# Optimization experiments

Measured on AMD Instinct MI355X. Metric: run time of the kernel, lower is better.

## Reference

```python
import jax, jax.numpy as jnp
import numpy as np

A = 180      # number of projection angles (theta = arange(180))
STEPS = 4    # partial-sum bands -> output has 1+STEPS channels


def _radon(x):
    # x: [N, 1, W, W]
    N, C, H, W = x.shape
    img = x[:, 0]  # [N, W, W]

    # --- affine grids for all angles (torch affine_grid, align_corners=False) ---
    thetas = jnp.arange(A, dtype=jnp.float32) * (jnp.pi / 180.0)
    c = jnp.cos(thetas)[:, None, None]   # [A,1,1]
    s = jnp.sin(thetas)[:, None, None]
    # align_corners=False base coords: centers of pixels in [-1, 1]
    base = ((jnp.arange(W, dtype=jnp.float32) + 0.5) * (2.0 / W)) - 1.0
    bx = base[None, None, :]             # [1,1,W] (x varies along last dim)
    by = base[None, :, None]             # [1,W,1] (y varies along rows)
    # R = [[cos, sin, 0], [-sin, cos, 0]]
    gx = c * bx + s * by                 # [A,W,W] normalized sample x
    gy = -s * bx + c * by                # [A,W,W] normalized sample y

    # --- bilinear grid_sample, padding_mode='zeros', align_corners=False ---
    ix = ((gx + 1.0) * W - 1.0) * 0.5
    iy = ((gy + 1.0) * W - 1.0) * 0.5
    x0 = jnp.floor(ix).astype(jnp.int32); x1 = x0 + 1
    y0 = jnp.floor(iy).astype(jnp.int32); y1 = y0 + 1
    wx1 = ix - x0; wx0 = 1.0 - wx1
    wy1 = iy - y0; wy0 = 1.0 - wy1

    def gather(yy, xx, w):
        valid = ((yy >= 0) & (yy < W) & (xx >= 0) & (xx < W)).astype(img.dtype)
        v = img[:, jnp.clip(yy, 0, W - 1), jnp.clip(xx, 0, W - 1)]  # [N,A,W,W]
        return v * (valid * w)[None]

    sampled = (gather(y0, x0, wy0 * wx0) + gather(y0, x1, wy0 * wx1)
               + gather(y1, x0, wy1 * wx0) + gather(y1, x1, wy1 * wx1))  # [N,A,W,W]

    # --- normalized hard masks: band of rows |row - center| < t, divided by band size ---
    segs = np.linspace(1, W / 2, STEPS + 1, dtype=int)
    ran = np.abs(np.arange(W) - (W - 1) / 2.0)
    wts = np.stack([(ran < t).astype(np.float32) / max((ran < t).sum(), 1)
                    for t in segs])  # [1+STEPS, W]

    # out[n, s, w, a] = sum_h sampled[n, a, h, w] * wts[s, h]
    return jnp.einsum('nahw,sh->nswa', sampled, jnp.asarray(wts))


def setup_inputs() -> dict:
    key = jax.random.key(0)
    x = jax.random.normal(key, (4, 1, 256, 256), dtype=jnp.float32)
    return {"x": x}


def reference(x):
    return _radon(x)
```

## Files before the change

### kernel.cpp

```cpp
#include <hip/hip_runtime.h>


constexpr int WIDTH  = 256;
constexpr int NANG   = 180;
constexpr int NBATCH = 4;
constexpr int NS     = 5;
constexpr int CSTR   = 131;
constexpr int ROWS   = 260;

typedef _Float16 h2 __attribute__((ext_vector_type(2)));

#if __has_builtin(__builtin_amdgcn_fractf)
#define FRACT(x) __builtin_amdgcn_fractf(x)
#else
#define FRACT(x) ((x) - floorf(x))
#endif

__device__ inline unsigned pack2_f16(float a, float b) {
    _Float16 ha = (_Float16)a, hb = (_Float16)b;
    unsigned short ua = __builtin_bit_cast(unsigned short, ha);
    unsigned short ub = __builtin_bit_cast(unsigned short, hb);
    return (unsigned)ua | ((unsigned)ub << 16);
}

__global__ __launch_bounds__(1024) void radon_kernel(const float* __restrict__ x,
                                                     float* __restrict__ out) {
    __shared__ unsigned cells[ROWS * CSTR];

    const int bid = blockIdx.x;
    const int lin = (bid & 7) * 90 + (bid >> 3);
    const int n = lin / NANG;
    const int a = lin - n * NANG;
    const int t = threadIdx.x;
    const int w = t & 255;
    const int quarter = t >> 8;

    const float* __restrict__ img = x + (size_t)n * WIDTH * WIDTH;

    const float theta = (float)a * 0.017453292519943295f;
    float s, c;
    sincosf(theta, &s, &c);
    const bool transp = (c * c > s * s);

    for (int i = t; i < 2 * CSTR; i += 1024) {
        cells[i] = 0u;
        cells[258 * CSTR + i] = 0u;
    }
    if (t < ROWS) {
        const int b = t * CSTR;
        cells[b] = 0u; cells[b + 129] = 0u; cells[b + 130] = 0u;
    }
    __syncthreads();

    if (!transp) {
        for (int d = t; d < 32768; d += 1024) {
            const int y = d >> 7, xd = d & 127;
            const float2 v = ((const float2*)img)[d];
            cells[(y + 2) * CSTR + xd + 1] = pack2_f16(v.x, v.y);
        }
    } else {
        for (int yp = quarter; yp < 128; yp += 4) {
            const float v0 = img[(2 * yp) * WIDTH + w];
            const float v1 = img[(2 * yp + 1) * WIDTH + w];
            cells[(w + 2) * CSTR + yp + 1] = pack2_f16(v0, v1);
        }
    }
    __syncthreads();

    const float bw  = ((float)w + 0.5f) * (2.0f / WIDTH) - 1.0f;
    const float bh0 = 0.5f * (2.0f / WIDTH) - 1.0f;
    const float gx0 = c * bw + s * bh0;
    const float gy0 = -s * bw + c * bh0;
    const float ix0 = ((gx0 + 1.0f) * (float)WIDTH - 1.0f) * 0.5f;
    const float iy0 = ((gy0 + 1.0f) * (float)WIDTH - 1.0f) * 0.5f;

    const float fast0 = (transp ? iy0 : ix0) + 2.0f;
    const float slow0 = (transp ? ix0 : iy0) + 2.0f;
    const float dfast = transp ? c : s;
    const float dslow = transp ? s : c;

    float r0 = 0.f, r1 = 0.f, r2 = 0.f, r3 = 0.f, r4 = 0.f;

    auto sample = [&](int h, float& r) {
        const float hf = (float)h;
        float fa = fmaf(hf, dfast, fast0);
        float sl = fmaf(hf, dslow, slow0);
        fa = __builtin_amdgcn_fmed3f(fa, 1.0f, 258.0f);
        sl = __builtin_amdgcn_fmed3f(sl, 1.0f, 258.0f);
        const int fi = (int)fa, si = (int)sl;
        const float wf = FRACT(fa);
        const float ws = FRACT(sl);
        const int j = fi >> 1;
        const int sh = (fi & 1) << 4;
        const unsigned* rowA = &cells[__mul24(si, CSTR) + j];
        const unsigned loA = rowA[0],    hiA = rowA[1];
        const unsigned loB = rowA[CSTR], hiB = rowA[CSTR + 1];
        const unsigned pa = __builtin_amdgcn_alignbit(hiA, loA, sh);
        const unsigned pb = __builtin_amdgcn_alignbit(hiB, loB, sh);
        const h2 va = __builtin_bit_cast(h2, pa);
        const h2 vb = __builtin_bit_cast(h2, pb);
        const _Float16 wsh = (_Float16)ws;
        const h2 ws2 = {wsh, wsh};
        const h2 col = (vb - va) * ws2 + va;
        const float c0 = (float)col.x;
        const float c1 = (float)col.y;
        r += fmaf(wf, c1 - c0, c0);
    };

    if (quarter == 0) {
        #pragma unroll 8
        for (int h = 0; h < 32; ++h)    sample(h, r4);
        #pragma unroll 8
        for (int h = 32; h < 64; ++h)   sample(h, r3);
    } else if (quarter == 1) {
        #pragma unroll 8
        for (int h = 64; h < 96; ++h)   sample(h, r2);
        #pragma unroll 8
        for (int h = 96; h < 127; ++h)  sample(h, r1);
        sample(127, r0);
    } else if (quarter == 2) {
        sample(128, r0);
        #pragma unroll 8
        for (int h = 129; h < 160; ++h) sample(h, r1);
        #pragma unroll 8
        for (int h = 160; h < 192; ++h) sample(h, r2);
    } else {
        #pragma unroll 8
        for (int h = 192; h < 224; ++h) sample(h, r3);
        #pragma unroll 8
        for (int h = 224; h < 256; ++h) sample(h, r4);
    }

    __syncthreads();
    float* red = (float*)cells;
    const int base = t * NS;
    red[base + 0] = r0;
    red[base + 1] = r1;
    red[base + 2] = r2;
    red[base + 3] = r3;
    red[base + 4] = r4;
    __syncthreads();

    if (t < 256) {
        const int b0 = t * NS, b1 = b0 + 256 * NS, b2 = b0 + 512 * NS, b3 = b0 + 768 * NS;
        const float s0 = (red[b0+0] + red[b1+0]) + (red[b2+0] + red[b3+0]);
        const float s1 = (red[b0+1] + red[b1+1]) + (red[b2+1] + red[b3+1]);
        const float s2 = (red[b0+2] + red[b1+2]) + (red[b2+2] + red[b3+2]);
        const float s3 = (red[b0+3] + red[b1+3]) + (red[b2+3] + red[b3+3]);
        const float s4 = (red[b0+4] + red[b1+4]) + (red[b2+4] + red[b3+4]);

        float* o = out + (((size_t)n * NS) * WIDTH + (size_t)t) * NANG + (size_t)a;
        float cum = s0;
        o[0]                          = cum * (1.0f / 2.0f);
        cum += s1;
        o[(size_t)1 * WIDTH * NANG]   = cum * (1.0f / 64.0f);
        cum += s2;
        o[(size_t)2 * WIDTH * NANG]   = cum * (1.0f / 128.0f);
        cum += s3;
        o[(size_t)3 * WIDTH * NANG]   = cum * (1.0f / 192.0f);
        cum += s4;
        o[(size_t)4 * WIDTH * NANG]   = cum * (1.0f / 256.0f);
    }
}

extern "C" void kernel_launch(void* const* d_in, const int* in_sizes, int n_in,
                              void* d_out, int out_size, void* d_ws, size_t ws_size,
                              hipStream_t stream) {
    const float* x = (const float*)d_in[0];
    float* out = (float*)d_out;
    radon_kernel<<<NBATCH * NANG, 1024, 0, stream>>>(x, out);
}
```

Measured before the change: 51.41 us.

## Split staged image into two half-height LDS passes to cut shared memory

Stages the fp16-packed image into LDS in two halves along the slow axis instead of all at once, which halves the shared-memory footprint so that more than one 1024-thread block can be resident per CU. Each pass computes a wavefront-uniform range of h whose samples fall into the staged half and masks out-of-half samples. It adds a second global load and staging phase, extra barriers, wave-level min/max shuffles and per-sample masking, and raises the launch-bounds occupancy hint.

After: 80.85 us. 1.57x slower.

```diff
diff --git a/kernel.cpp b/kernel.cpp
--- a/kernel.cpp
+++ b/kernel.cpp
@@ -6,7 +6,8 @@
 constexpr int NBATCH = 4;
 constexpr int NS     = 5;
 constexpr int CSTR   = 131;
-constexpr int ROWS   = 260;
+constexpr int LROWS  = 131;
+constexpr int SPLIT  = 130;
 
 typedef _Float16 h2 __attribute__((ext_vector_type(2)));
 
@@ -23,9 +24,9 @@
     return (unsigned)ua | ((unsigned)ub << 16);
 }
 
-__global__ __launch_bounds__(1024) void radon_kernel(const float* __restrict__ x,
-                                                     float* __restrict__ out) {
-    __shared__ unsigned cells[ROWS * CSTR];
+__global__ __launch_bounds__(1024, 8) void radon_kernel(const float* __restrict__ x,
+                                                        float* __restrict__ out) {
+    __shared__ unsigned cells[LROWS * CSTR];
 
     const int bid = blockIdx.x;
     const int lin = (bid & 7) * 90 + (bid >> 3);
@@ -42,31 +43,6 @@
     sincosf(theta, &s, &c);
     const bool transp = (c * c > s * s);
 
-    for (int i = t; i < 2 * CSTR; i += 1024) {
-        cells[i] = 0u;
-        cells[258 * CSTR + i] = 0u;
-    }
-    if (t < ROWS) {
-        const int b = t * CSTR;
-        cells[b] = 0u; cells[b + 129] = 0u; cells[b + 130] = 0u;
-    }
-    __syncthreads();
-
-    if (!transp) {
-        for (int d = t; d < 32768; d += 1024) {
-            const int y = d >> 7, xd = d & 127;
-            const float2 v = ((const float2*)img)[d];
-            cells[(y + 2) * CSTR + xd + 1] = pack2_f16(v.x, v.y);
-        }
-    } else {
-        for (int yp = quarter; yp < 128; yp += 4) {
-            const float v0 = img[(2 * yp) * WIDTH + w];
-            const float v1 = img[(2 * yp + 1) * WIDTH + w];
-            cells[(w + 2) * CSTR + yp + 1] = pack2_f16(v0, v1);
-        }
-    }
-    __syncthreads();
-
     const float bw  = ((float)w + 0.5f) * (2.0f / WIDTH) - 1.0f;
     const float bh0 = 0.5f * (2.0f / WIDTH) - 1.0f;
     const float gx0 = c * bw + s * bh0;
@@ -81,57 +57,113 @@
 
     float r0 = 0.f, r1 = 0.f, r2 = 0.f, r3 = 0.f, r4 = 0.f;
 
-    auto sample = [&](int h, float& r) {
-        const float hf = (float)h;
-        float fa = fmaf(hf, dfast, fast0);
-        float sl = fmaf(hf, dslow, slow0);
-        fa = __builtin_amdgcn_fmed3f(fa, 1.0f, 258.0f);
-        sl = __builtin_amdgcn_fmed3f(sl, 1.0f, 258.0f);
-        const int fi = (int)fa, si = (int)sl;
-        const float wf = FRACT(fa);
-        const float ws = FRACT(sl);
-        const int j = fi >> 1;
-        const int sh = (fi & 1) << 4;
-        const unsigned* rowA = &cells[__mul24(si, CSTR) + j];
-        const unsigned loA = rowA[0],    hiA = rowA[1];
-        const unsigned loB = rowA[CSTR], hiB = rowA[CSTR + 1];
-        const unsigned pa = __builtin_amdgcn_alignbit(hiA, loA, sh);
-        const unsigned pb = __builtin_amdgcn_alignbit(hiB, loB, sh);
-        const h2 va = __builtin_bit_cast(h2, pa);
-        const h2 vb = __builtin_bit_cast(h2, pb);
-        const _Float16 wsh = (_Float16)ws;
-        const h2 ws2 = {wsh, wsh};
-        const h2 col = (vb - va) * ws2 + va;
-        const float c0 = (float)col.x;
-        const float c1 = (float)col.y;
-        r += fmaf(wf, c1 - c0, c0);
-    };
-
-    if (quarter == 0) {
-        #pragma unroll 8
-        for (int h = 0; h < 32; ++h)    sample(h, r4);
-        #pragma unroll 8
-        for (int h = 32; h < 64; ++h)   sample(h, r3);
-    } else if (quarter == 1) {
-        #pragma unroll 8
-        for (int h = 64; h < 96; ++h)   sample(h, r2);
-        #pragma unroll 8
-        for (int h = 96; h < 127; ++h)  sample(h, r1);
-        sample(127, r0);
-    } else if (quarter == 2) {
-        sample(128, r0);
-        #pragma unroll 8
-        for (int h = 129; h < 160; ++h) sample(h, r1);
-        #pragma unroll 8
-        for (int h = 160; h < 192; ++h) sample(h, r2);
-    } else {
-        #pragma unroll 8
-        for (int h = 192; h < 224; ++h) sample(h, r3);
-        #pragma unroll 8
-        for (int h = 224; h < 256; ++h) sample(h, r4);
+    for (int pass = 0; pass < 2; ++pass) {
+        if (t < LROWS) {
+            const int b = t * CSTR;
+            cells[b] = 0u; cells[b + 129] = 0u; cells[b + 130] = 0u;
+        }
+        if (pass == 0) {
+            for (int i = t; i < 2 * CSTR; i += 1024) cells[i] = 0u;
+        } else {
+            for (int i = t; i < 3 * CSTR; i += 1024) cells[128 * CSTR + i] = 0u;
+        }
+
+        if (!transp) {
+            const int nrows = pass ? 128 : 129;
+            const int glo   = pass ? 128 : 0;
+            for (int d = t; d < nrows * 128; d += 1024) {
+                const int ys = d >> 7, xd = d & 127;
+                const float2 v = ((const float2*)img)[(glo + ys) * 128 + xd];
+                const int loc = pass ? ys : (ys + 2);
+                cells[loc * CSTR + xd + 1] = pack2_f16(v.x, v.y);
+            }
+        } else {
+            const bool part = pass ? (w >= 128) : (w <= 128);
+            if (part) {
+                const int loc = pass ? (w - 128) : (w + 2);
+                for (int yp = quarter; yp < 128; yp += 4) {
+                    const float v0 = img[(2 * yp) * WIDTH + w];
+                    const float v1 = img[(2 * yp + 1) * WIDTH + w];
+                    cells[loc * CSTR + yp + 1] = pack2_f16(v0, v1);
+                }
+            }
+        }
+        __syncthreads();
+
+        const float hstar = (130.0f - slow0) / dslow;
+        const float hcl = fminf(fmaxf(hstar, -10000.0f), 10000.0f);
+        int lo, hi;
+        if (dslow > 0.0f) {
+            if (pass == 0) { lo = 0;            hi = (int)hcl + 3; }
+            else           { lo = (int)hcl - 3; hi = 256; }
+        } else if (dslow < 0.0f) {
+            if (pass == 0) { lo = (int)hcl - 3; hi = 256; }
+            else           { lo = 0;            hi = (int)hcl + 3; }
+        } else { lo = 0; hi = 256; }
+        lo = max(lo, 0); hi = min(hi, 256);
+
+        int wlo = lo, whi = hi;
+        for (int off = 1; off < 64; off <<= 1) {
+            wlo = min(wlo, __shfl_xor(wlo, off));
+            whi = max(whi, __shfl_xor(whi, off));
+        }
+        wlo = __builtin_amdgcn_readfirstlane(wlo);
+        whi = __builtin_amdgcn_readfirstlane(whi);
+
+        auto sample = [&](int h) -> float {
+            const float hf = (float)h;
+            float fa = fmaf(hf, dfast, fast0);
+            float sl = fmaf(hf, dslow, slow0);
+            fa = __builtin_amdgcn_fmed3f(fa, 1.0f, 258.0f);
+            sl = __builtin_amdgcn_fmed3f(sl, 1.0f, 258.0f);
+            const bool m = (sl < 130.0f) == (pass == 0);
+            const int fi = (int)fa, si = (int)sl;
+            const float wf = FRACT(fa);
+            const float ws = FRACT(sl);
+            const int j = fi >> 1;
+            const int sh = (fi & 1) << 4;
+            int siL = si - SPLIT * pass;
+            siL = min(max(siL, 0), 129);
+            const unsigned* rowA = &cells[__mul24(siL, CSTR) + j];
+            const unsigned loA = rowA[0],    hiA = rowA[1];
+            const unsigned loB = rowA[CSTR], hiB = rowA[CSTR + 1];
+            const unsigned pa = __builtin_amdgcn_alignbit(hiA, loA, sh);
+            const unsigned pb = __builtin_amdgcn_alignbit(hiB, loB, sh);
+            const h2 va = __builtin_bit_cast(h2, pa);
+            const h2 vb = __builtin_bit_cast(h2, pb);
+            const _Float16 wsh = (_Float16)ws;
+            const h2 ws2 = {wsh, wsh};
+            const h2 col = (vb - va) * ws2 + va;
+            const float c0 = (float)col.x;
+            const float c1 = (float)col.y;
+            const float val = fmaf(wf, c1 - c0, c0);
+            return m ? val : 0.0f;
+        };
+
+        #define SEG(LO, HI, R) { \
+            const int hs = max(LO, wlo), he = min(HI, whi); \
+            _Pragma("unroll 8") \
+            for (int h = hs; h < he; ++h) R += sample(h); }
+        if (quarter == 0) {
+            SEG(0, 32, r4)
+            SEG(32, 64, r3)
+        } else if (quarter == 1) {
+            SEG(64, 96, r2)
+            SEG(96, 127, r1)
+            if (127 >= wlo && 127 < whi) r0 += sample(127);
+        } else if (quarter == 2) {
+            if (128 >= wlo && 128 < whi) r0 += sample(128);
+            SEG(129, 160, r1)
+            SEG(160, 192, r2)
+        } else {
+            SEG(192, 224, r3)
+            SEG(224, 256, r4)
+        }
+        #undef SEG
+
+        __syncthreads();
     }
 
-    __syncthreads();
     float* red = (float*)cells;
     const int base = t * NS;
     red[base + 0] = r0;
```
